# Optimization experiments

Hardware: AMD Instinct MI355X
Metric: run time of the kernel (lower is better)

## Reference

```python
import jax, jax.numpy as jnp
import numpy as np

H_IMG, W_IMG, N_GAUSS = 256, 256, 512


def setup_inputs() -> dict:
    key = jax.random.key(0)
    k1, k2, k3, k4 = jax.random.split(key, 4)
    # Gaussian centers uniformly inside the image (pixel coords)
    means_2d = jax.random.uniform(k1, (N_GAUSS, 2), dtype=jnp.float32) * jnp.array([W_IMG, H_IMG], dtype=jnp.float32)
    # SPD 2x2 covariances: A A^T + eps*I, scaled to a few-pixel footprint
    A = jax.random.normal(k2, (N_GAUSS, 2, 2), dtype=jnp.float32) * 3.0
    cov_2d = jnp.einsum('nij,nkj->nik', A, A) + 0.3 * jnp.eye(2, dtype=jnp.float32)[None]
    opacities = jax.random.uniform(k3, (N_GAUSS,), dtype=jnp.float32)
    colors = jax.random.uniform(k4, (N_GAUSS, 3), dtype=jnp.float32)
    return {"means_2d": means_2d, "cov_2d": cov_2d, "opacities": opacities,
            "colors": colors, "H": H_IMG, "W": W_IMG}


def reference(means_2d, cov_2d, opacities, colors, H, W):
    # pixel centers [H, W, 2] in (x, y) order, +0.5 center offset
    gy, gx = jnp.meshgrid(jnp.arange(H), jnp.arange(W), indexing='ij')
    pix = jnp.stack([gx, gy], axis=-1).astype(jnp.float32) + 0.5

    # analytic 2x2 inverse of each covariance
    a, b = cov_2d[:, 0, 0], cov_2d[:, 0, 1]
    c, d = cov_2d[:, 1, 0], cov_2d[:, 1, 1]
    det = a * d - b * c
    inv_cov = jnp.stack([jnp.stack([d, -b], axis=-1),
                         jnp.stack([-c, a], axis=-1)], axis=-2) / det[:, None, None]  # [N,2,2]

    dx = pix[:, :, None, :] - means_2d[None, None, :, :]            # [H,W,N,2]
    intermediate = jnp.einsum('hwnk,nkl->hwnl', dx, inv_cov)        # [H,W,N,2]
    mahalanobis = jnp.sum(intermediate * dx, axis=-1)               # [H,W,N]
    gaussian_weight = jnp.exp(-0.5 * mahalanobis)

    alpha = opacities[None, None, :] * gaussian_weight              # [H,W,N]
    cumprod = jnp.cumprod(1.0 - alpha + 1e-7, axis=-1)
    transmittance = jnp.concatenate(
        [jnp.ones((H, W, 1), dtype=alpha.dtype), cumprod[:, :, :-1]], axis=-1)
    weights = alpha * transmittance
    rendered = jnp.einsum('hwn,nc->hwc', weights, colors)           # [H,W,3]
    return rendered
```

## Files before the change

kernel.cpp:

```cpp
#include <hip/hip_runtime.h>
#include <hip/hip_bf16.h>

#ifndef __has_builtin
#define __has_builtin(x) 0
#endif

__device__ __forceinline__ float fast_exp2(float x) {
#if __has_builtin(__builtin_amdgcn_exp2f)
  return __builtin_amdgcn_exp2f(x);
#else
  return exp2f(x);
#endif
}
__device__ __forceinline__ float fast_rcp(float x) {
#if __has_builtin(__builtin_amdgcn_rcpf)
  return __builtin_amdgcn_rcpf(x);
#else
  return 1.0f / x;
#endif
}

#define NG     512
#define NSEG   8
#define SEGLEN 64
#define PXB    128
#define QCUT   -21.0f

__global__ __launch_bounds__(512, 4) void render_kernel(
    const float* __restrict__ means, const float* __restrict__ cov,
    const float* __restrict__ opac,  const float* __restrict__ cols,
    float* __restrict__ out)
{
  __shared__ float4 sp[NG * 3];
  __shared__ float4 part[NSEG][PXB];
  __shared__ float  outstage[PXB * 3];

  const int tid = threadIdx.x;

  {
    const int g = tid;
    const float mx = means[2*g], my = means[2*g+1];
    const float a = cov[4*g+0], b = cov[4*g+1], c = cov[4*g+2], d = cov[4*g+3];
    const float inv = 1.0f / (a*d - b*c);
    const float HL2E = 0.72134752f;
    const float ka = -HL2E * d * inv;
    const float kb =  HL2E * (b + c) * inv;
    const float kc = -HL2E * a * inv;
    const float ko = log2f(opac[g]);
    sp[3*g+0] = make_float4(mx, my, ka, kb);
    sp[3*g+1] = make_float4(kc, ko, cols[3*g+0], cols[3*g+1]);
    sp[3*g+2] = make_float4(cols[3*g+2], 0.f, 0.f, 0.f);
  }
  __syncthreads();

  const int lane = tid & 63;
  const int seg  = tid >> 6;
  const int pixbase = blockIdx.x * PXB;
  const float py  = (float)(pixbase >> 8) + 0.5f;
  const float x0f = (float)(pixbase & 255) + 0.5f;
  const float px0 = x0f + (float)lane;

  unsigned long long mask;
  {
    const int gt = seg * SEGLEN + lane;
    const float4 q0 = sp[3*gt+0];
    const float4 q1 = sp[3*gt+1];
    const float dy = py - q0.y;
    const float B  = q0.w * dy;
    const float cc = fmaf(q1.x * dy, dy, q1.y);
    const float lo = x0f - q0.x;
    const float hi = lo + 127.0f;
    float dxs = B * (-0.5f * fast_rcp(q0.z));
    dxs = fminf(fmaxf(dxs, lo), hi);
    const float q = fmaf(fmaf(q0.z, dxs, B), dxs, cc);
    mask = __ballot(q > QCUT);
  }

  float T0 = 1.f, T1 = 1.f;
  float r0 = 0.f, g0 = 0.f, b0 = 0.f, r1 = 0.f, g1 = 0.f, b1 = 0.f;
  while (mask) {
    const int bit = __ffsll(mask) - 1;
    mask &= mask - 1;
    const int g = seg * SEGLEN + bit;
    const float4 q0 = sp[3*g+0];
    const float4 q1 = sp[3*g+1];
    const float4 q2 = sp[3*g+2];
    const float dy   = py - q0.y;
    const float kbdy = q0.w * dy;
    const float v    = fmaf(q1.x * dy, dy, q1.y);
    const float dx0  = px0 - q0.x;
    const float dx1  = dx0 + 64.0f;
    const float m0 = fmaf(fmaf(q0.z, dx0, kbdy), dx0, v);
    const float m1 = fmaf(fmaf(q0.z, dx1, kbdy), dx1, v);
    const float a0 = fast_exp2(m0);
    const float a1 = fast_exp2(m1);
    const float aw0 = a0 * T0;
    const float aw1 = a1 * T1;
    r0 = fmaf(aw0, q1.z, r0); g0 = fmaf(aw0, q1.w, g0); b0 = fmaf(aw0, q2.x, b0);
    r1 = fmaf(aw1, q1.z, r1); g1 = fmaf(aw1, q1.w, g1); b1 = fmaf(aw1, q2.x, b1);
    T0 *= (1.0000001f - a0);
    T1 *= (1.0000001f - a1);
  }

  part[seg][lane]      = make_float4(r0, g0, b0, T0);
  part[seg][lane + 64] = make_float4(r1, g1, b1, T1);
  __syncthreads();

  if (tid < PXB) {
    float T = 1.f, R = 0.f, G = 0.f, B = 0.f;
#pragma unroll
    for (int s = 0; s < NSEG; ++s) {
      const float4 p = part[s][tid];
      R = fmaf(T, p.x, R);
      G = fmaf(T, p.y, G);
      B = fmaf(T, p.z, B);
      T *= p.w;
    }
    outstage[tid*3+0] = R;
    outstage[tid*3+1] = G;
    outstage[tid*3+2] = B;
  }
  __syncthreads();

  if (tid < PXB * 3) {
    out[pixbase * 3 + tid] = outstage[tid];
  }
}

extern "C" void kernel_launch(void* const* d_in, const int* in_sizes, int n_in,
                              void* d_out, int out_size, void* d_ws, size_t ws_size,
                              hipStream_t stream) {
  const float* means = (const float*)d_in[0];
  const float* cov   = (const float*)d_in[1];
  const float* opac  = (const float*)d_in[2];
  const float* cols  = (const float*)d_in[3];
  float* out = (float*)d_out;
  (void)in_sizes; (void)n_in; (void)out_size; (void)d_ws; (void)ws_size;
  render_kernel<<<dim3(256 * 256 / PXB), dim3(512), 0, stream>>>(
      means, cov, opac, cols, out);
}
```

Baseline: 65.04 us.

## Precompute gaussian params in a prep kernel and cache per-row coefficients in LDS

```diff
diff --git a/kernel.cpp b/kernel.cpp
--- a/kernel.cpp
+++ b/kernel.cpp
@@ -1,5 +1,4 @@
 #include <hip/hip_runtime.h>
-#include <hip/hip_bf16.h>
 
 #ifndef __has_builtin
 #define __has_builtin(x) 0
@@ -26,31 +25,40 @@
 #define PXB    128
 #define QCUT   -21.0f
 
-__global__ __launch_bounds__(512, 4) void render_kernel(
+__global__ __launch_bounds__(NG, 1) void prep_kernel(
     const float* __restrict__ means, const float* __restrict__ cov,
     const float* __restrict__ opac,  const float* __restrict__ cols,
-    float* __restrict__ out)
+    float4* __restrict__ ws)
 {
-  __shared__ float4 sp[NG * 3];
+  const int g = threadIdx.x;
+  const float mx = means[2*g], my = means[2*g+1];
+  const float a = cov[4*g+0], b = cov[4*g+1], c = cov[4*g+2], d = cov[4*g+3];
+  const float inv = 1.0f / (a*d - b*c);
+  const float HL2E = 0.72134752f;
+  const float ka = -HL2E * d * inv;
+  const float kb =  HL2E * (b + c) * inv;
+  const float kc = -HL2E * a * inv;
+  const float ko = log2f(opac[g]);
+  ws[g]        = make_float4(mx, my, ka, kb);
+  ws[NG + g]   = make_float4(kc, ko, 0.f, 0.f);
+  ws[2*NG + g] = make_float4(cols[3*g+0], cols[3*g+1], cols[3*g+2], 0.f);
+}
+
+__global__ __launch_bounds__(512, 4) void render_kernel(
+    const float4* __restrict__ ws, float* __restrict__ out)
+{
+  __shared__ float4 arrA[NG];
+  __shared__ float4 arrB[NG];
+  __shared__ float4 colp[NG];
+  __shared__ float4 rowp[NG];
   __shared__ float4 part[NSEG][PXB];
   __shared__ float  outstage[PXB * 3];
 
   const int tid = threadIdx.x;
 
-  {
-    const int g = tid;
-    const float mx = means[2*g], my = means[2*g+1];
-    const float a = cov[4*g+0], b = cov[4*g+1], c = cov[4*g+2], d = cov[4*g+3];
-    const float inv = 1.0f / (a*d - b*c);
-    const float HL2E = 0.72134752f;
-    const float ka = -HL2E * d * inv;
-    const float kb =  HL2E * (b + c) * inv;
-    const float kc = -HL2E * a * inv;
-    const float ko = log2f(opac[g]);
-    sp[3*g+0] = make_float4(mx, my, ka, kb);
-    sp[3*g+1] = make_float4(kc, ko, cols[3*g+0], cols[3*g+1]);
-    sp[3*g+2] = make_float4(cols[3*g+2], 0.f, 0.f, 0.f);
-  }
+  arrA[tid] = ws[tid];
+  arrB[tid] = ws[NG + tid];
+  colp[tid] = ws[2*NG + tid];
   __syncthreads();
 
   const int lane = tid & 63;
@@ -63,16 +71,17 @@
   unsigned long long mask;
   {
     const int gt = seg * SEGLEN + lane;
-    const float4 q0 = sp[3*gt+0];
-    const float4 q1 = sp[3*gt+1];
-    const float dy = py - q0.y;
-    const float B  = q0.w * dy;
-    const float cc = fmaf(q1.x * dy, dy, q1.y);
-    const float lo = x0f - q0.x;
+    const float4 A  = arrA[gt];
+    const float4 Bq = arrB[gt];
+    const float dy = py - A.y;
+    const float Bv = A.w * dy;
+    const float cc = fmaf(Bq.x * dy, dy, Bq.y);
+    rowp[gt] = make_float4(A.x, A.z, Bv, cc);
+    const float lo = x0f - A.x;
     const float hi = lo + 127.0f;
-    float dxs = B * (-0.5f * fast_rcp(q0.z));
+    float dxs = Bv * (-0.5f * fast_rcp(A.z));
     dxs = fminf(fmaxf(dxs, lo), hi);
-    const float q = fmaf(fmaf(q0.z, dxs, B), dxs, cc);
+    const float q = fmaf(fmaf(A.z, dxs, Bv), dxs, cc);
     mask = __ballot(q > QCUT);
   }
 
@@ -82,22 +91,18 @@
     const int bit = __ffsll(mask) - 1;
     mask &= mask - 1;
     const int g = seg * SEGLEN + bit;
-    const float4 q0 = sp[3*g+0];
-    const float4 q1 = sp[3*g+1];
-    const float4 q2 = sp[3*g+2];
-    const float dy   = py - q0.y;
-    const float kbdy = q0.w * dy;
-    const float v    = fmaf(q1.x * dy, dy, q1.y);
-    const float dx0  = px0 - q0.x;
-    const float dx1  = dx0 + 64.0f;
-    const float m0 = fmaf(fmaf(q0.z, dx0, kbdy), dx0, v);
-    const float m1 = fmaf(fmaf(q0.z, dx1, kbdy), dx1, v);
+    const float4 P = rowp[g];
+    const float4 C = colp[g];
+    const float dx0 = px0 - P.x;
+    const float dx1 = dx0 + 64.0f;
+    const float m0 = fmaf(fmaf(P.y, dx0, P.z), dx0, P.w);
+    const float m1 = fmaf(fmaf(P.y, dx1, P.z), dx1, P.w);
     const float a0 = fast_exp2(m0);
     const float a1 = fast_exp2(m1);
     const float aw0 = a0 * T0;
     const float aw1 = a1 * T1;
-    r0 = fmaf(aw0, q1.z, r0); g0 = fmaf(aw0, q1.w, g0); b0 = fmaf(aw0, q2.x, b0);
-    r1 = fmaf(aw1, q1.z, r1); g1 = fmaf(aw1, q1.w, g1); b1 = fmaf(aw1, q2.x, b1);
+    r0 = fmaf(aw0, C.x, r0); g0 = fmaf(aw0, C.y, g0); b0 = fmaf(aw0, C.z, b0);
+    r1 = fmaf(aw1, C.x, r1); g1 = fmaf(aw1, C.y, g1); b1 = fmaf(aw1, C.z, b1);
     T0 *= (1.0000001f - a0);
     T1 *= (1.0000001f - a1);
   }
@@ -135,7 +140,8 @@
   const float* opac  = (const float*)d_in[2];
   const float* cols  = (const float*)d_in[3];
   float* out = (float*)d_out;
-  (void)in_sizes; (void)n_in; (void)out_size; (void)d_ws; (void)ws_size;
-  render_kernel<<<dim3(256 * 256 / PXB), dim3(512), 0, stream>>>(
-      means, cov, opac, cols, out);
+  float4* ws = (float4*)d_ws;
+  (void)in_sizes; (void)n_in; (void)out_size; (void)ws_size;
+  prep_kernel<<<dim3(1), dim3(NG), 0, stream>>>(means, cov, opac, cols, ws);
+  render_kernel<<<dim3(256 * 256 / PXB), dim3(512), 0, stream>>>(ws, out);
 }
```

After: 66.11 us. About the same (+1.6%).
